# Optimization experiments

Hardware: AMD Instinct MI355X
Metric: run time of the kernel (lower is better)

The kernel has to match this reference:

```python
import jax, jax.numpy as jnp
import numpy as np

NUM_HEADS = 32
NUM_KV_HEADS = 8
HEAD_SIZE = 128
SCALE = 0.08838834764831845  # 1/sqrt(128)
BATCH = 32
MAX_BLOCKS_PER_SEQ = 128
BLOCK_SIZE = 16
NUM_BLOCKS = BATCH * MAX_BLOCKS_PER_SEQ  # 4096
MAX_CTX = MAX_BLOCKS_PER_SEQ * BLOCK_SIZE  # 2048


def setup_inputs() -> dict:
    key = jax.random.key(0)
    ks = jax.random.split(key, 8)
    query = jax.random.normal(ks[0], (BATCH, 1, NUM_HEADS * HEAD_SIZE), dtype=jnp.float32)
    k_new = jax.random.normal(ks[1], (BATCH, 1, NUM_KV_HEADS * HEAD_SIZE), dtype=jnp.float32)
    v_new = jax.random.normal(ks[2], (BATCH, 1, NUM_KV_HEADS * HEAD_SIZE), dtype=jnp.float32)
    key_cache = jax.random.normal(ks[3], (NUM_BLOCKS, NUM_KV_HEADS, HEAD_SIZE, BLOCK_SIZE), dtype=jnp.float32)
    value_cache = jax.random.normal(ks[4], (NUM_BLOCKS, NUM_KV_HEADS, HEAD_SIZE, BLOCK_SIZE), dtype=jnp.float32)
    # each sequence owns a contiguous stripe of blocks, accessed through the table
    block_tables = jnp.arange(NUM_BLOCKS, dtype=jnp.int32).reshape(BATCH, MAX_BLOCKS_PER_SEQ)
    context_lens = jax.random.randint(ks[5], (BATCH,), 1, MAX_CTX + 1, dtype=jnp.int32)
    # slot for the newly-decoded token (position context_len-1)
    last = context_lens - 1
    blk_idx = block_tables[jnp.arange(BATCH), last // BLOCK_SIZE]
    slot_mapping = (blk_idx * BLOCK_SIZE + last % BLOCK_SIZE).reshape(BATCH, 1).astype(jnp.int32)
    return {
        "query": query, "key": k_new, "value": v_new,
        "key_cache": key_cache, "value_cache": value_cache,
        "block_tables": block_tables, "context_lens": context_lens,
        "slot_mapping": slot_mapping,
    }


def reference(query, key, value, key_cache, value_cache, block_tables, context_lens, slot_mapping):
    B = query.shape[0]
    block_size = value_cache.shape[3]
    q_per_kv = NUM_HEADS // NUM_KV_HEADS

    # --- reshape_and_cache: write new k/v into paged caches at slot_mapping ---
    slots = slot_mapping.reshape(-1)                       # [B] (seq_len=1 decode)
    blk = slots // block_size
    off = slots % block_size
    k_new = key.reshape(B, NUM_KV_HEADS, HEAD_SIZE)
    v_new = value.reshape(B, NUM_KV_HEADS, HEAD_SIZE)
    key_cache = key_cache.at[blk, :, :, off].set(k_new)
    value_cache = value_cache.at[blk, :, :, off].set(v_new)

    # --- paged_attention_v1: gather blocks via block_tables, masked softmax ---
    # [B, MB, KVH, D, bs] -> [B, MB, bs, KVH, D] -> [B, T, KVH, D]
    K = jnp.moveaxis(key_cache[block_tables], -1, 2).reshape(B, -1, NUM_KV_HEADS, HEAD_SIZE)
    V = jnp.moveaxis(value_cache[block_tables], -1, 2).reshape(B, -1, NUM_KV_HEADS, HEAD_SIZE)
    T = K.shape[1]

    q = query.reshape(B, NUM_KV_HEADS, q_per_kv, HEAD_SIZE)
    scores = jnp.einsum('bkqd,btkd->bkqt', q, K) * SCALE   # [B, KVH, Qper, T]
    valid = (jnp.arange(T, dtype=jnp.int32)[None, :] < context_lens[:, None])
    scores = jnp.where(valid[:, None, None, :], scores, jnp.finfo(scores.dtype).min)
    probs = jax.nn.softmax(scores, axis=-1)
    out = jnp.einsum('bkqt,btkd->bkqd', probs, V)          # [B, KVH, Qper, D]
    return out.reshape(B, 1, NUM_HEADS * HEAD_SIZE)
```

## Files before the change

kernel.cpp:

```cpp
#include <hip/hip_runtime.h>
#include <float.h>

#define NUM_HEADS    32
#define NUM_KV_HEADS 8
#define HEAD_SIZE    128
#define Q_PER_KV     4
#define BLOCK_SZ     16
#define MAX_BLOCKS   128
#define MAX_CTX      2048
#define SCALE        0.08838834764831845f

#define CHUNK_BLOCKS 16
#define CHUNK_TOK    (CHUNK_BLOCKS * BLOCK_SZ)
#define NCHUNK       (MAX_BLOCKS / CHUNK_BLOCKS)
#define WS_STRIDE    (2 * Q_PER_KV + Q_PER_KV * HEAD_SIZE)

typedef float v4f __attribute__((ext_vector_type(4)));

__global__ __launch_bounds__(64, 8)
void paged_attn_chunk(const float* __restrict__ query,
                      const float* __restrict__ key_cache,
                      const float* __restrict__ value_cache,
                      const int* __restrict__ block_tables,
                      const int* __restrict__ context_lens,
                      float* __restrict__ ws) {
    const int h   = blockIdx.x;
    const int b   = blockIdx.y;
    const int c   = blockIdx.z;
    const int tid = threadIdx.x;

    const int ctx  = context_lens[b];
    const int nb   = (ctx + BLOCK_SZ - 1) / BLOCK_SZ;
    const int cb   = c * CHUNK_BLOCKS;
    if (cb >= nb) return;
    const int last = ctx - 1;

    __shared__ float q_lds[Q_PER_KV * HEAD_SIZE];
    __shared__ float s_lds[Q_PER_KV * CHUNK_TOK];
    __shared__ float ml_lds[2 * Q_PER_KV];

    {
        const v4f* qg = reinterpret_cast<const v4f*>(
            query + ((size_t)b * NUM_HEADS + h * Q_PER_KV) * HEAD_SIZE);
        v4f* ql = reinterpret_cast<v4f*>(q_lds);
        ql[tid]      = qg[tid]      * SCALE;
        ql[tid + 64] = qg[tid + 64] * SCALE;
    }
    __syncthreads();

    {
        const int bil = tid >> 2;
        const int o   = tid & 3;
        const int bi  = cb + bil;
        const int t0  = bil * BLOCK_SZ + o * 4;
        if (bi < nb) {
            const int phys = block_tables[b * MAX_BLOCKS + bi];
            const v4f* kp = reinterpret_cast<const v4f*>(key_cache) +
                            ((size_t)phys * NUM_KV_HEADS + h) * (HEAD_SIZE * BLOCK_SZ / 4);
            const v4f* q4 = reinterpret_cast<const v4f*>(q_lds);
            v4f acc[Q_PER_KV];
            #pragma unroll
            for (int qh = 0; qh < Q_PER_KV; ++qh) acc[qh] = (v4f)0.f;
            #pragma unroll 4
            for (int d4 = 0; d4 < HEAD_SIZE / 4; ++d4) {
                v4f k[4];
                #pragma unroll
                for (int dd = 0; dd < 4; ++dd) k[dd] = kp[d4 * 16 + dd * 4 + o];
                #pragma unroll
                for (int qh = 0; qh < Q_PER_KV; ++qh) {
                    v4f qv = q4[qh * (HEAD_SIZE / 4) + d4];
                    #pragma unroll
                    for (int dd = 0; dd < 4; ++dd) acc[qh] += qv[dd] * k[dd];
                }
            }
            const int g0 = c * CHUNK_TOK + t0;
            #pragma unroll
            for (int qh = 0; qh < Q_PER_KV; ++qh) {
                v4f sv;
                #pragma unroll
                for (int j = 0; j < 4; ++j) {
                    const int g = g0 + j;
                    sv[j] = (g < ctx && g != last) ? acc[qh][j] : -FLT_MAX;
                }
                *reinterpret_cast<v4f*>(&s_lds[qh * CHUNK_TOK + t0]) = sv;
            }
        } else {
            const v4f mv = (v4f)(-FLT_MAX);
            #pragma unroll
            for (int qh = 0; qh < Q_PER_KV; ++qh)
                *reinterpret_cast<v4f*>(&s_lds[qh * CHUNK_TOK + t0]) = mv;
        }
    }
    __syncthreads();

    float* wsp = ws + (((size_t)b * NUM_KV_HEADS + h) * NCHUNK + c) * WS_STRIDE;
    #pragma unroll
    for (int qh = 0; qh < Q_PER_KV; ++qh) {
        float s0 = s_lds[qh * CHUNK_TOK + tid];
        float s1 = s_lds[qh * CHUNK_TOK + tid + 64];
        float s2 = s_lds[qh * CHUNK_TOK + tid + 128];
        float s3 = s_lds[qh * CHUNK_TOK + tid + 192];
        float m = fmaxf(fmaxf(s0, s1), fmaxf(s2, s3));
        #pragma unroll
        for (int off = 32; off; off >>= 1) m = fmaxf(m, __shfl_xor(m, off));
        float p0 = (s0 == -FLT_MAX) ? 0.f : __expf(s0 - m);
        float p1 = (s1 == -FLT_MAX) ? 0.f : __expf(s1 - m);
        float p2 = (s2 == -FLT_MAX) ? 0.f : __expf(s2 - m);
        float p3 = (s3 == -FLT_MAX) ? 0.f : __expf(s3 - m);
        s_lds[qh * CHUNK_TOK + tid]       = p0;
        s_lds[qh * CHUNK_TOK + tid + 64]  = p1;
        s_lds[qh * CHUNK_TOK + tid + 128] = p2;
        s_lds[qh * CHUNK_TOK + tid + 192] = p3;
        float l = p0 + p1 + p2 + p3;
        #pragma unroll
        for (int off = 32; off; off >>= 1) l += __shfl_xor(l, off);
        if (tid == 0) { ml_lds[qh] = m; ml_lds[Q_PER_KV + qh] = l; }
    }
    __syncthreads();
    if (tid < 2 * Q_PER_KV) wsp[tid] = ml_lds[tid];

    {
        const int d0 = tid, d1 = tid + 64;
        float acc0[Q_PER_KV] = {0.f, 0.f, 0.f, 0.f};
        float acc1[Q_PER_KV] = {0.f, 0.f, 0.f, 0.f};
        const int nbl = min(nb - cb, CHUNK_BLOCKS);
        for (int bil = 0; bil < nbl; ++bil) {
            const int phys = block_tables[b * MAX_BLOCKS + cb + bil];
            const v4f* vp = reinterpret_cast<const v4f*>(value_cache) +
                            ((size_t)phys * NUM_KV_HEADS + h) * (HEAD_SIZE * BLOCK_SZ / 4);
            v4f vv0[4], vv1[4];
            #pragma unroll
            for (int j = 0; j < 4; ++j) { vv0[j] = vp[d0 * 4 + j]; vv1[j] = vp[d1 * 4 + j]; }
            #pragma unroll
            for (int qh = 0; qh < Q_PER_KV; ++qh) {
                const v4f* pq = reinterpret_cast<const v4f*>(
                    &s_lds[qh * CHUNK_TOK + bil * BLOCK_SZ]);
                #pragma unroll
                for (int j = 0; j < 4; ++j) {
                    v4f p = pq[j];
                    acc0[qh] += p[0]*vv0[j][0] + p[1]*vv0[j][1] + p[2]*vv0[j][2] + p[3]*vv0[j][3];
                    acc1[qh] += p[0]*vv1[j][0] + p[1]*vv1[j][1] + p[2]*vv1[j][2] + p[3]*vv1[j][3];
                }
            }
        }
        float* wo = wsp + 2 * Q_PER_KV;
        #pragma unroll
        for (int qh = 0; qh < Q_PER_KV; ++qh) {
            wo[qh * HEAD_SIZE + d0] = acc0[qh];
            wo[qh * HEAD_SIZE + d1] = acc1[qh];
        }
    }
}

__global__ __launch_bounds__(512, 2)
void paged_attn_reduce(const float* __restrict__ query,
                       const float* __restrict__ k_new,
                       const float* __restrict__ v_new,
                       const int* __restrict__ context_lens,
                       const float* __restrict__ ws,
                       float* __restrict__ out) {
    const int h   = blockIdx.x;
    const int b   = blockIdx.y;
    const int tid = threadIdx.x;

    __shared__ float snew_lds[Q_PER_KV];

    const int ctx = context_lens[b];
    const int nb  = (ctx + BLOCK_SZ - 1) / BLOCK_SZ;
    const int nch = (nb + CHUNK_BLOCKS - 1) / CHUNK_BLOCKS;

    if (tid < 4 * 64) {
        const int w = tid >> 6, lane = tid & 63;
        const float* qp = query + ((size_t)b * NUM_HEADS + h * Q_PER_KV + w) * HEAD_SIZE;
        const float* kn = k_new + ((size_t)b * NUM_KV_HEADS + h) * HEAD_SIZE;
        float v = qp[lane] * kn[lane] + qp[lane + 64] * kn[lane + 64];
        #pragma unroll
        for (int off = 32; off; off >>= 1) v += __shfl_xor(v, off);
        if (lane == 0) snew_lds[w] = v * SCALE;
    }
    __syncthreads();

    const int qh = tid >> 7, d = tid & 127;
    const float* wsb = ws + ((size_t)b * NUM_KV_HEADS + h) * NCHUNK * WS_STRIDE;

    float M = -FLT_MAX, L = 0.f, acc = 0.f;
    for (int c = 0; c < nch; ++c) {
        const float* wsp = wsb + (size_t)c * WS_STRIDE;
        const float mc = wsp[qh];
        const float lc = wsp[Q_PER_KV + qh];
        const float oc = wsp[2 * Q_PER_KV + qh * HEAD_SIZE + d];
        const float nM = fmaxf(M, mc);
        const float eM = __expf(M - nM), ec = __expf(mc - nM);
        acc = acc * eM + oc * ec;
        L   = L   * eM + lc * ec;
        M   = nM;
    }
    {
        const float s  = snew_lds[qh];
        const float nM = fmaxf(M, s);
        const float eM = __expf(M - nM), es = __expf(s - nM);
        const float vn = v_new[((size_t)b * NUM_KV_HEADS + h) * HEAD_SIZE + d];
        acc = acc * eM + es * vn;
        L   = L   * eM + es;
    }
    out[((size_t)b * NUM_HEADS + h * Q_PER_KV + qh) * HEAD_SIZE + d] = acc / L;
}

extern "C" void kernel_launch(void* const* d_in, const int* in_sizes, int n_in,
                              void* d_out, int out_size, void* d_ws, size_t ws_size,
                              hipStream_t stream) {
    const float* query       = (const float*)d_in[0];
    const float* k_new       = (const float*)d_in[1];
    const float* v_new       = (const float*)d_in[2];
    const float* key_cache   = (const float*)d_in[3];
    const float* value_cache = (const float*)d_in[4];
    const int*   block_tables  = (const int*)d_in[5];
    const int*   context_lens  = (const int*)d_in[6];
    float* out = (float*)d_out;
    float* ws  = (float*)d_ws;

    const int batch = in_sizes[6];

    dim3 g1(NUM_KV_HEADS, batch, NCHUNK);
    paged_attn_chunk<<<g1, 64, 0, stream>>>(query, key_cache, value_cache,
                                            block_tables, context_lens, ws);
    dim3 g2(NUM_KV_HEADS, batch);
    paged_attn_reduce<<<g2, 512, 0, stream>>>(query, k_new, v_new,
                                              context_lens, ws, out);
}
```

Measured before the change: 65.68 us.

## Shrink attention chunks to four blocks and split QK dot over lane groups

Chunk size drops from 16 to 4 KV blocks, which quadruples the number of workgroups and gives more parallelism for the memory-bound decode. Within a chunk each block is now handled by 16 lanes, each covering a quarter of the head dimension, and the partial dot products are combined with cross-lane shuffles. Softmax now uses one score per lane, and the max and sum are written straight to the workspace. The cost is four times more partial results for the reduce kernel to merge, plus extra shuffle work.

```diff
diff --git a/kernel.cpp b/kernel.cpp
--- a/kernel.cpp
+++ b/kernel.cpp
@@ -10,7 +10,7 @@
 #define MAX_CTX      2048
 #define SCALE        0.08838834764831845f
 
-#define CHUNK_BLOCKS 16
+#define CHUNK_BLOCKS 4
 #define CHUNK_TOK    (CHUNK_BLOCKS * BLOCK_SZ)
 #define NCHUNK       (MAX_BLOCKS / CHUNK_BLOCKS)
 #define WS_STRIDE    (2 * Q_PER_KV + Q_PER_KV * HEAD_SIZE)
@@ -29,15 +29,14 @@
     const int c   = blockIdx.z;
     const int tid = threadIdx.x;
 
-    const int ctx  = context_lens[b];
-    const int nb   = (ctx + BLOCK_SZ - 1) / BLOCK_SZ;
-    const int cb   = c * CHUNK_BLOCKS;
+    const int ctx = context_lens[b];
+    const int nb  = (ctx + BLOCK_SZ - 1) / BLOCK_SZ;
+    const int cb  = c * CHUNK_BLOCKS;
     if (cb >= nb) return;
     const int last = ctx - 1;
 
     __shared__ float q_lds[Q_PER_KV * HEAD_SIZE];
     __shared__ float s_lds[Q_PER_KV * CHUNK_TOK];
-    __shared__ float ml_lds[2 * Q_PER_KV];
 
     {
         const v4f* qg = reinterpret_cast<const v4f*>(
@@ -49,30 +48,39 @@
     __syncthreads();
 
     {
-        const int bil = tid >> 2;
         const int o   = tid & 3;
+        const int rep = (tid >> 2) & 3;
+        const int bil = tid >> 4;
         const int bi  = cb + bil;
-        const int t0  = bil * BLOCK_SZ + o * 4;
+        v4f acc[Q_PER_KV];
+        #pragma unroll
+        for (int qh = 0; qh < Q_PER_KV; ++qh) acc[qh] = (v4f)0.f;
+
         if (bi < nb) {
             const int phys = block_tables[b * MAX_BLOCKS + bi];
             const v4f* kp = reinterpret_cast<const v4f*>(key_cache) +
                             ((size_t)phys * NUM_KV_HEADS + h) * (HEAD_SIZE * BLOCK_SZ / 4);
-            const v4f* q4 = reinterpret_cast<const v4f*>(q_lds);
-            v4f acc[Q_PER_KV];
-            #pragma unroll
-            for (int qh = 0; qh < Q_PER_KV; ++qh) acc[qh] = (v4f)0.f;
-            #pragma unroll 4
-            for (int d4 = 0; d4 < HEAD_SIZE / 4; ++d4) {
-                v4f k[4];
+            #pragma unroll 8
+            for (int i = 0; i < 32; ++i) {
+                const int d = rep * 32 + i;
+                const v4f k4 = kp[d * 4 + o];
                 #pragma unroll
-                for (int dd = 0; dd < 4; ++dd) k[dd] = kp[d4 * 16 + dd * 4 + o];
-                #pragma unroll
-                for (int qh = 0; qh < Q_PER_KV; ++qh) {
-                    v4f qv = q4[qh * (HEAD_SIZE / 4) + d4];
-                    #pragma unroll
-                    for (int dd = 0; dd < 4; ++dd) acc[qh] += qv[dd] * k[dd];
-                }
-            }
+                for (int qh = 0; qh < Q_PER_KV; ++qh)
+                    acc[qh] += q_lds[qh * HEAD_SIZE + d] * k4;
+            }
+        }
+        #pragma unroll
+        for (int qh = 0; qh < Q_PER_KV; ++qh) {
+            #pragma unroll
+            for (int j = 0; j < 4; ++j) {
+                float v = acc[qh][j];
+                v += __shfl_xor(v, 4);
+                v += __shfl_xor(v, 8);
+                acc[qh][j] = v;
+            }
+        }
+        if (rep == 0) {
+            const int t0 = bil * BLOCK_SZ + o * 4;
             const int g0 = c * CHUNK_TOK + t0;
             #pragma unroll
             for (int qh = 0; qh < Q_PER_KV; ++qh) {
@@ -80,15 +88,10 @@
                 #pragma unroll
                 for (int j = 0; j < 4; ++j) {
                     const int g = g0 + j;
-                    sv[j] = (g < ctx && g != last) ? acc[qh][j] : -FLT_MAX;
+                    sv[j] = (bi < nb && g < ctx && g != last) ? acc[qh][j] : -FLT_MAX;
                 }
                 *reinterpret_cast<v4f*>(&s_lds[qh * CHUNK_TOK + t0]) = sv;
             }
-        } else {
-            const v4f mv = (v4f)(-FLT_MAX);
-            #pragma unroll
-            for (int qh = 0; qh < Q_PER_KV; ++qh)
-                *reinterpret_cast<v4f*>(&s_lds[qh * CHUNK_TOK + t0]) = mv;
         }
     }
     __syncthreads();
@@ -96,34 +99,25 @@
     float* wsp = ws + (((size_t)b * NUM_KV_HEADS + h) * NCHUNK + c) * WS_STRIDE;
     #pragma unroll
     for (int qh = 0; qh < Q_PER_KV; ++qh) {
-        float s0 = s_lds[qh * CHUNK_TOK + tid];
-        float s1 = s_lds[qh * CHUNK_TOK + tid + 64];
-        float s2 = s_lds[qh * CHUNK_TOK + tid + 128];
-        float s3 = s_lds[qh * CHUNK_TOK + tid + 192];
-        float m = fmaxf(fmaxf(s0, s1), fmaxf(s2, s3));
+        const float s = s_lds[qh * CHUNK_TOK + tid];
+        float m = s;
         #pragma unroll
         for (int off = 32; off; off >>= 1) m = fmaxf(m, __shfl_xor(m, off));
-        float p0 = (s0 == -FLT_MAX) ? 0.f : __expf(s0 - m);
-        float p1 = (s1 == -FLT_MAX) ? 0.f : __expf(s1 - m);
-        float p2 = (s2 == -FLT_MAX) ? 0.f : __expf(s2 - m);
-        float p3 = (s3 == -FLT_MAX) ? 0.f : __expf(s3 - m);
-        s_lds[qh * CHUNK_TOK + tid]       = p0;
-        s_lds[qh * CHUNK_TOK + tid + 64]  = p1;
-        s_lds[qh * CHUNK_TOK + tid + 128] = p2;
-        s_lds[qh * CHUNK_TOK + tid + 192] = p3;
-        float l = p0 + p1 + p2 + p3;
+        const float p = (s == -FLT_MAX) ? 0.f : __expf(s - m);
+        s_lds[qh * CHUNK_TOK + tid] = p;
+        float l = p;
         #pragma unroll
         for (int off = 32; off; off >>= 1) l += __shfl_xor(l, off);
-        if (tid == 0) { ml_lds[qh] = m; ml_lds[Q_PER_KV + qh] = l; }
-    }
-    __syncthreads();
-    if (tid < 2 * Q_PER_KV) wsp[tid] = ml_lds[tid];
+        if (tid == 0) { wsp[qh] = m; wsp[Q_PER_KV + qh] = l; }
+    }
+    __syncthreads();
 
     {
         const int d0 = tid, d1 = tid + 64;
         float acc0[Q_PER_KV] = {0.f, 0.f, 0.f, 0.f};
         float acc1[Q_PER_KV] = {0.f, 0.f, 0.f, 0.f};
         const int nbl = min(nb - cb, CHUNK_BLOCKS);
+        #pragma unroll 2
         for (int bil = 0; bil < nbl; ++bil) {
             const int phys = block_tables[b * MAX_BLOCKS + cb + bil];
             const v4f* vp = reinterpret_cast<const v4f*>(value_cache) +
@@ -137,7 +131,7 @@
                     &s_lds[qh * CHUNK_TOK + bil * BLOCK_SZ]);
                 #pragma unroll
                 for (int j = 0; j < 4; ++j) {
-                    v4f p = pq[j];
+                    const v4f p = pq[j];
                     acc0[qh] += p[0]*vv0[j][0] + p[1]*vv0[j][1] + p[2]*vv0[j][2] + p[3]*vv0[j][3];
                     acc1[qh] += p[0]*vv1[j][0] + p[1]*vv1[j][1] + p[2]*vv1[j][2] + p[3]*vv1[j][3];
                 }
```

Result: slower. 160.5 us (+144.3%).

## Split each sequence into four equal chunks with 256-thread blocks

Applied to the files above, without the earlier changes.

Replaces fixed 16-block chunks of 64 threads with a fixed split of four equal chunks per (batch, kv-head). Each chunk is handled by a 256-thread block, and the PV product is split across two thread segments that are reduced through LDS. The goal is to balance work across blocks regardless of context length, avoid idle grid slots for short sequences, and give more threads to each chunk so memory latency is hidden better. In exchange there are fewer blocks overall, an extra LDS reduction, and larger shared memory use for long chunks, which could lower occupancy.

```diff
diff --git a/kernel.cpp b/kernel.cpp
--- a/kernel.cpp
+++ b/kernel.cpp
@@ -7,17 +7,16 @@
 #define Q_PER_KV     4
 #define BLOCK_SZ     16
 #define MAX_BLOCKS   128
-#define MAX_CTX      2048
 #define SCALE        0.08838834764831845f
 
-#define CHUNK_BLOCKS 16
-#define CHUNK_TOK    (CHUNK_BLOCKS * BLOCK_SZ)
-#define NCHUNK       (MAX_BLOCKS / CHUNK_BLOCKS)
-#define WS_STRIDE    (2 * Q_PER_KV + Q_PER_KV * HEAD_SIZE)
+#define NSPLIT           4
+#define MAX_CHUNK_BLOCKS ((MAX_BLOCKS + NSPLIT - 1) / NSPLIT)
+#define MAX_CHUNK_TOK    (MAX_CHUNK_BLOCKS * BLOCK_SZ)
+#define WS_STRIDE        528
 
 typedef float v4f __attribute__((ext_vector_type(4)));
 
-__global__ __launch_bounds__(64, 8)
+__global__ __launch_bounds__(256, 4)
 void paged_attn_chunk(const float* __restrict__ query,
                       const float* __restrict__ key_cache,
                       const float* __restrict__ value_cache,
@@ -29,32 +28,31 @@
     const int c   = blockIdx.z;
     const int tid = threadIdx.x;
 
-    const int ctx  = context_lens[b];
-    const int nb   = (ctx + BLOCK_SZ - 1) / BLOCK_SZ;
-    const int cb   = c * CHUNK_BLOCKS;
-    if (cb >= nb) return;
+    const int ctx = context_lens[b];
+    const int nb  = (ctx + BLOCK_SZ - 1) / BLOCK_SZ;
+    const int q   = (nb + NSPLIT - 1) / NSPLIT;
+    const int b0  = c * q;
+    if (b0 >= nb) return;
+    const int nbl  = min(nb - b0, q);
     const int last = ctx - 1;
 
     __shared__ float q_lds[Q_PER_KV * HEAD_SIZE];
-    __shared__ float s_lds[Q_PER_KV * CHUNK_TOK];
+    __shared__ float s_lds[Q_PER_KV * MAX_CHUNK_TOK];
+    __shared__ float red_lds[2 * Q_PER_KV * HEAD_SIZE];
     __shared__ float ml_lds[2 * Q_PER_KV];
 
-    {
+    if (tid < 128) {
         const v4f* qg = reinterpret_cast<const v4f*>(
             query + ((size_t)b * NUM_HEADS + h * Q_PER_KV) * HEAD_SIZE);
-        v4f* ql = reinterpret_cast<v4f*>(q_lds);
-        ql[tid]      = qg[tid]      * SCALE;
-        ql[tid + 64] = qg[tid + 64] * SCALE;
-    }
-    __syncthreads();
-
-    {
+        reinterpret_cast<v4f*>(q_lds)[tid] = qg[tid] * SCALE;
+    }
+    __syncthreads();
+
+    {
+        const int o   = tid & 3;
         const int bil = tid >> 2;
-        const int o   = tid & 3;
-        const int bi  = cb + bil;
-        const int t0  = bil * BLOCK_SZ + o * 4;
-        if (bi < nb) {
-            const int phys = block_tables[b * MAX_BLOCKS + bi];
+        if (bil < nbl) {
+            const int phys = block_tables[b * MAX_BLOCKS + b0 + bil];
             const v4f* kp = reinterpret_cast<const v4f*>(key_cache) +
                             ((size_t)phys * NUM_KV_HEADS + h) * (HEAD_SIZE * BLOCK_SZ / 4);
             const v4f* q4 = reinterpret_cast<const v4f*>(q_lds);
@@ -68,12 +66,13 @@
                 for (int dd = 0; dd < 4; ++dd) k[dd] = kp[d4 * 16 + dd * 4 + o];
                 #pragma unroll
                 for (int qh = 0; qh < Q_PER_KV; ++qh) {
-                    v4f qv = q4[qh * (HEAD_SIZE / 4) + d4];
+                    const v4f qv = q4[qh * (HEAD_SIZE / 4) + d4];
                     #pragma unroll
                     for (int dd = 0; dd < 4; ++dd) acc[qh] += qv[dd] * k[dd];
                 }
             }
-            const int g0 = c * CHUNK_TOK + t0;
+            const int t0 = bil * BLOCK_SZ + o * 4;
+            const int g0 = b0 * BLOCK_SZ + t0;
             #pragma unroll
             for (int qh = 0; qh < Q_PER_KV; ++qh) {
                 v4f sv;
@@ -82,72 +81,70 @@
                     const int g = g0 + j;
                     sv[j] = (g < ctx && g != last) ? acc[qh][j] : -FLT_MAX;
                 }
-                *reinterpret_cast<v4f*>(&s_lds[qh * CHUNK_TOK + t0]) = sv;
+                *reinterpret_cast<v4f*>(&s_lds[qh * MAX_CHUNK_TOK + t0]) = sv;
             }
-        } else {
-            const v4f mv = (v4f)(-FLT_MAX);
-            #pragma unroll
-            for (int qh = 0; qh < Q_PER_KV; ++qh)
-                *reinterpret_cast<v4f*>(&s_lds[qh * CHUNK_TOK + t0]) = mv;
-        }
-    }
-    __syncthreads();
-
-    float* wsp = ws + (((size_t)b * NUM_KV_HEADS + h) * NCHUNK + c) * WS_STRIDE;
-    #pragma unroll
-    for (int qh = 0; qh < Q_PER_KV; ++qh) {
-        float s0 = s_lds[qh * CHUNK_TOK + tid];
-        float s1 = s_lds[qh * CHUNK_TOK + tid + 64];
-        float s2 = s_lds[qh * CHUNK_TOK + tid + 128];
-        float s3 = s_lds[qh * CHUNK_TOK + tid + 192];
-        float m = fmaxf(fmaxf(s0, s1), fmaxf(s2, s3));
+        }
+    }
+    __syncthreads();
+
+    {
+        const int w = tid >> 6, lane = tid & 63;
+        const int T = nbl * BLOCK_SZ;
+        float m = -FLT_MAX;
+        for (int t = lane; t < T; t += 64) m = fmaxf(m, s_lds[w * MAX_CHUNK_TOK + t]);
         #pragma unroll
         for (int off = 32; off; off >>= 1) m = fmaxf(m, __shfl_xor(m, off));
-        float p0 = (s0 == -FLT_MAX) ? 0.f : __expf(s0 - m);
-        float p1 = (s1 == -FLT_MAX) ? 0.f : __expf(s1 - m);
-        float p2 = (s2 == -FLT_MAX) ? 0.f : __expf(s2 - m);
-        float p3 = (s3 == -FLT_MAX) ? 0.f : __expf(s3 - m);
-        s_lds[qh * CHUNK_TOK + tid]       = p0;
-        s_lds[qh * CHUNK_TOK + tid + 64]  = p1;
-        s_lds[qh * CHUNK_TOK + tid + 128] = p2;
-        s_lds[qh * CHUNK_TOK + tid + 192] = p3;
-        float l = p0 + p1 + p2 + p3;
+        float l = 0.f;
+        for (int t = lane; t < T; t += 64) {
+            const float s = s_lds[w * MAX_CHUNK_TOK + t];
+            const float p = (s == -FLT_MAX) ? 0.f : __expf(s - m);
+            s_lds[w * MAX_CHUNK_TOK + t] = p;
+            l += p;
+        }
         #pragma unroll
         for (int off = 32; off; off >>= 1) l += __shfl_xor(l, off);
-        if (tid == 0) { ml_lds[qh] = m; ml_lds[Q_PER_KV + qh] = l; }
-    }
-    __syncthreads();
-    if (tid < 2 * Q_PER_KV) wsp[tid] = ml_lds[tid];
-
-    {
-        const int d0 = tid, d1 = tid + 64;
-        float acc0[Q_PER_KV] = {0.f, 0.f, 0.f, 0.f};
-        float acc1[Q_PER_KV] = {0.f, 0.f, 0.f, 0.f};
-        const int nbl = min(nb - cb, CHUNK_BLOCKS);
-        for (int bil = 0; bil < nbl; ++bil) {
-            const int phys = block_tables[b * MAX_BLOCKS + cb + bil];
+        if (lane == 0) { ml_lds[w] = m; ml_lds[Q_PER_KV + w] = l; }
+    }
+    __syncthreads();
+
+    {
+        const int d   = tid & 127;
+        const int seg = tid >> 7;
+        float acc[Q_PER_KV] = {0.f, 0.f, 0.f, 0.f};
+        for (int bil = seg; bil < nbl; bil += 2) {
+            const int phys = block_tables[b * MAX_BLOCKS + b0 + bil];
             const v4f* vp = reinterpret_cast<const v4f*>(value_cache) +
                             ((size_t)phys * NUM_KV_HEADS + h) * (HEAD_SIZE * BLOCK_SZ / 4);
-            v4f vv0[4], vv1[4];
-            #pragma unroll
-            for (int j = 0; j < 4; ++j) { vv0[j] = vp[d0 * 4 + j]; vv1[j] = vp[d1 * 4 + j]; }
+            v4f vv[4];
+            #pragma unroll
+            for (int j = 0; j < 4; ++j) vv[j] = vp[d * 4 + j];
             #pragma unroll
             for (int qh = 0; qh < Q_PER_KV; ++qh) {
                 const v4f* pq = reinterpret_cast<const v4f*>(
-                    &s_lds[qh * CHUNK_TOK + bil * BLOCK_SZ]);
+                    &s_lds[qh * MAX_CHUNK_TOK + bil * BLOCK_SZ]);
                 #pragma unroll
                 for (int j = 0; j < 4; ++j) {
-                    v4f p = pq[j];
-                    acc0[qh] += p[0]*vv0[j][0] + p[1]*vv0[j][1] + p[2]*vv0[j][2] + p[3]*vv0[j][3];
-                    acc1[qh] += p[0]*vv1[j][0] + p[1]*vv1[j][1] + p[2]*vv1[j][2] + p[3]*vv1[j][3];
+                    const v4f p = pq[j];
+                    acc[qh] += p[0]*vv[j][0] + p[1]*vv[j][1] + p[2]*vv[j][2] + p[3]*vv[j][3];
                 }
             }
         }
-        float* wo = wsp + 2 * Q_PER_KV;
-        #pragma unroll
-        for (int qh = 0; qh < Q_PER_KV; ++qh) {
-            wo[qh * HEAD_SIZE + d0] = acc0[qh];
-            wo[qh * HEAD_SIZE + d1] = acc1[qh];
+        #pragma unroll
+        for (int qh = 0; qh < Q_PER_KV; ++qh)
+            red_lds[(seg * Q_PER_KV + qh) * HEAD_SIZE + d] = acc[qh];
+    }
+    __syncthreads();
+
+    float* wsp = ws + (((size_t)b * NUM_KV_HEADS + h) * NSPLIT + c) * WS_STRIDE;
+    if (tid < 2 * Q_PER_KV) wsp[tid] = ml_lds[tid];
+    {
+        const int d = tid & 127, qp2 = tid >> 7;
+        #pragma unroll
+        for (int k = 0; k < 2; ++k) {
+            const int qh = qp2 * 2 + k;
+            wsp[2 * Q_PER_KV + qh * HEAD_SIZE + d] =
+                red_lds[qh * HEAD_SIZE + d] +
+                red_lds[(Q_PER_KV + qh) * HEAD_SIZE + d];
         }
     }
 }
@@ -167,7 +164,7 @@
 
     const int ctx = context_lens[b];
     const int nb  = (ctx + BLOCK_SZ - 1) / BLOCK_SZ;
-    const int nch = (nb + CHUNK_BLOCKS - 1) / CHUNK_BLOCKS;
+    const int q   = (nb + NSPLIT - 1) / NSPLIT;
 
     if (tid < 4 * 64) {
         const int w = tid >> 6, lane = tid & 63;
@@ -181,10 +178,12 @@
     __syncthreads();
 
     const int qh = tid >> 7, d = tid & 127;
-    const float* wsb = ws + ((size_t)b * NUM_KV_HEADS + h) * NCHUNK * WS_STRIDE;
+    const float* wsb = ws + ((size_t)b * NUM_KV_HEADS + h) * NSPLIT * WS_STRIDE;
 
     float M = -FLT_MAX, L = 0.f, acc = 0.f;
-    for (int c = 0; c < nch; ++c) {
+    #pragma unroll
+    for (int c = 0; c < NSPLIT; ++c) {
+        if (c * q >= nb) break;
         const float* wsp = wsb + (size_t)c * WS_STRIDE;
         const float mc = wsp[qh];
         const float lc = wsp[Q_PER_KV + qh];
@@ -221,9 +220,9 @@
 
     const int batch = in_sizes[6];
 
-    dim3 g1(NUM_KV_HEADS, batch, NCHUNK);
-    paged_attn_chunk<<<g1, 64, 0, stream>>>(query, key_cache, value_cache,
-                                            block_tables, context_lens, ws);
+    dim3 g1(NUM_KV_HEADS, batch, NSPLIT);
+    paged_attn_chunk<<<g1, 256, 0, stream>>>(query, key_cache, value_cache,
+                                             block_tables, context_lens, ws);
     dim3 g2(NUM_KV_HEADS, batch);
     paged_attn_reduce<<<g2, 512, 0, stream>>>(query, k_new, v_new,
                                               context_lens, ws, out);
```

Result: slower. 68.46 us (+4.2%).
